# Kernel tuning notes

Hardware: AMD Instinct MI355X
Metric: run time of the kernel (lower is better)

## Reference

```python
import jax, jax.numpy as jnp
import numpy as np

T_TX, T_RX = 2, 2
NUM_VERTICES = 900
NUM_TRIANGLES = 400
ORDER = 2
NUM_PATH_CANDIDATES = 2048
EPSILON = 1e-6
HIT_THRESHOLD = 0.999


def setup_inputs() -> dict:
    key = jax.random.key(0)
    k1, k2, k3, k4, k5 = jax.random.split(key, 5)
    transmitters = jax.random.normal(k1, (T_TX, 3), dtype=jnp.float32) * 10.0
    receivers = jax.random.normal(k2, (T_RX, 3), dtype=jnp.float32) * 10.0
    vertices = jax.random.normal(k3, (NUM_VERTICES, 3), dtype=jnp.float32) * 5.0
    # Build triangles with three distinct vertex indices to avoid degenerate normals.
    i0 = jax.random.randint(k4, (NUM_TRIANGLES,), 0, NUM_VERTICES)
    triangles = jnp.stack([i0, (i0 + 7) % NUM_VERTICES, (i0 + 131) % NUM_VERTICES], axis=-1)
    tv = vertices[triangles]  # [Nt, 3, 3]
    n = jnp.cross(tv[:, 1] - tv[:, 0], tv[:, 2] - tv[:, 0])
    normals = n / jnp.linalg.norm(n, axis=-1, keepdims=True)  # unit plane normals, [Nt, 3]
    path_candidates = jax.random.randint(k5, (NUM_PATH_CANDIDATES, ORDER), 0, NUM_TRIANGLES)
    return {
        "transmitters": transmitters,
        "receivers": receivers,
        "vertices": vertices,
        "normals": normals,
        "triangles": triangles,
        "path_candidates": path_candidates,
    }


def image_method(from_v, to_v, mirror_vertices, mirror_normals):
    """from_v [T,1,1,3], to_v [1,R,1,3], mirrors [P,order,3] -> paths [T,R,P,order,3]."""
    num_mirrors = mirror_vertices.shape[-2]
    # Forward pass: successive mirror images of the transmitter.
    images = []
    cur = from_v
    for i in range(num_mirrors):
        mv = mirror_vertices[..., i, :]
        mn = mirror_normals[..., i, :]
        cur = cur - 2.0 * jnp.sum((cur - mv) * mn, axis=-1, keepdims=True) * mn
        images.append(cur)
    # Backward pass: intersect segment (image_i -> current point) with mirror plane i.
    pts = []
    cur = to_v
    for i in reversed(range(num_mirrors)):
        mv = mirror_vertices[..., i, :]
        mn = mirror_normals[..., i, :]
        img = images[i]
        u = cur - img
        t = jnp.sum((mv - img) * mn, axis=-1, keepdims=True) / jnp.sum(u * mn, axis=-1, keepdims=True)
        cur = img + t * u
        pts.append(cur)
    return jnp.stack(pts[::-1], axis=-2)


def triangles_contain_vertices(triangle_vertices, v):
    """triangle_vertices [P,order,3,3], v [T,R,P,order,3] -> bool [T,R,P,order]."""
    u0 = triangle_vertices[..., 0, :] - v
    u1 = triangle_vertices[..., 1, :] - v
    u2 = triangle_vertices[..., 2, :] - v
    n0 = jnp.cross(u0, u1)
    n1 = jnp.cross(u1, u2)
    n2 = jnp.cross(u2, u0)
    d01 = jnp.sum(n0 * n1, axis=-1)
    d12 = jnp.sum(n1 * n2, axis=-1)
    d20 = jnp.sum(n2 * n0, axis=-1)
    return (d01 >= 0.0) & (d12 >= 0.0) & (d20 >= 0.0)


def consecutive_same_side(full_paths, mirror_vertices, mirror_normals):
    """full_paths [T,R,P,order+2,3] -> bool [T,R,P,order]."""
    v_prev = full_paths[..., :-2, :]
    v_next = full_paths[..., 2:, :]
    d_prev = jnp.sum((v_prev - mirror_vertices) * mirror_normals, axis=-1)
    d_next = jnp.sum((v_next - mirror_vertices) * mirror_normals, axis=-1)
    return (d_prev * d_next) >= 0.0


def rays_intersect_any_triangle(ray_origins, ray_directions, triangle_vertices,
                                epsilon=EPSILON, hit_threshold=HIT_THRESHOLD):
    """Moller-Trumbore: rays [...,3] vs all triangles [Nt,3,3] -> bool [...]."""
    v0 = triangle_vertices[..., 0, :]
    e1 = triangle_vertices[..., 1, :] - v0
    e2 = triangle_vertices[..., 2, :] - v0
    ro = ray_origins[..., None, :]   # [..., Nt, 3] after broadcast
    rd = ray_directions[..., None, :]
    h = jnp.cross(rd, e2)
    a = jnp.sum(e1 * h, axis=-1)
    f = 1.0 / a
    s = ro - v0
    u = f * jnp.sum(s * h, axis=-1)
    q = jnp.cross(s, e1)
    v = f * jnp.sum(rd * q, axis=-1)
    t = f * jnp.sum(e2 * q, axis=-1)
    hit = (jnp.abs(a) > epsilon) & (u >= 0.0) & (u <= 1.0) & (v >= 0.0) \
        & (u + v <= 1.0) & (t > epsilon) & (t < hit_threshold)
    return hit.any(axis=-1)


def reference(transmitters, receivers, vertices, normals, triangles, path_candidates):
    from_v = transmitters.reshape(-1, 3)  # [T, 3]
    to_v = receivers.reshape(-1, 3)       # [R, 3]
    n_tx, n_rx = from_v.shape[0], to_v.shape[0]
    num_pc, order = path_candidates.shape

    tri = jnp.take(triangles, path_candidates, axis=0)          # [P, order, 3]
    triangle_vertices = jnp.take(vertices, tri, axis=0)          # [P, order, 3, 3]
    mirror_vertices = triangle_vertices[..., 0, :]               # [P, order, 3]
    mirror_normals = jnp.take(normals, path_candidates, axis=0)  # [P, order, 3]

    paths = image_method(from_v[:, None, None, :], to_v[None, :, None, :],
                         mirror_vertices, mirror_normals)        # [T,R,P,order,3]

    mask_1 = triangles_contain_vertices(triangle_vertices, paths).all(axis=-1)

    full_paths = jnp.concatenate(
        (
            jnp.broadcast_to(from_v[:, None, None, None, :], (n_tx, n_rx, num_pc, 1, 3)),
            paths,
            jnp.broadcast_to(to_v[None, :, None, None, :], (n_tx, n_rx, num_pc, 1, 3)),
        ),
        axis=-2,
    )  # [T,R,P,order+2,3]

    mask_2 = consecutive_same_side(full_paths, mirror_vertices, mirror_normals).all(axis=-1)

    ray_origins = full_paths[..., :-1, :]           # [T,R,P,order+1,3]
    ray_directions = jnp.diff(full_paths, axis=-2)  # [T,R,P,order+1,3]
    all_triangle_vertices = jnp.take(vertices, triangles, axis=0)  # [Nt,3,3]
    intersect = rays_intersect_any_triangle(ray_origins, ray_directions,
                                            all_triangle_vertices).any(axis=-1)
    mask_3 = ~intersect

    mask = mask_1 & mask_2 & mask_3  # [T,R,P]

    object_dtype = path_candidates.dtype
    tx_objects = jnp.broadcast_to(jnp.arange(n_tx, dtype=object_dtype)[:, None, None, None],
                                  (n_tx, n_rx, num_pc, 1))
    rx_objects = jnp.broadcast_to(jnp.arange(n_rx, dtype=object_dtype)[None, :, None, None],
                                  (n_tx, n_rx, num_pc, 1))
    pc = jnp.broadcast_to(path_candidates, (n_tx, n_rx, num_pc, order))
    objects = jnp.concatenate((tx_objects, pc, rx_objects), axis=-1)  # [T,R,P,order+2]

    return full_paths, objects, mask
```

## Files before the change

kernel.cpp:

```cpp
#include <hip/hip_runtime.h>

#pragma clang fp contract(off)

namespace {

constexpr int kT  = 2;
constexpr int kR  = 2;
constexpr int kP  = 2048;
constexpr int kNT = 400;
constexpr float kEps   = 1e-6f;
constexpr float kHitTh = 0.999f;

constexpr int kNumPaths  = kT * kR * kP;
constexpr int kFpFloats  = kNumPaths * 12;
constexpr int kObjFloats = kNumPaths * 4;

constexpr int kPathsPerBlock = 64;
constexpr int kBlocks = kNumPaths / kPathsPerBlock;

__device__ inline void cross3(const float a[3], const float b[3], float o[3]) {
    o[0] = a[1] * b[2] - a[2] * b[1];
    o[1] = a[2] * b[0] - a[0] * b[2];
    o[2] = a[0] * b[1] - a[1] * b[0];
}
__device__ inline float dot3(const float a[3], const float b[3]) {
    return a[0] * b[0] + a[1] * b[1] + a[2] * b[2];
}

__global__ __launch_bounds__(256)
void fused_kernel(const float* __restrict__ tx,
                  const float* __restrict__ rx,
                  const float* __restrict__ verts,
                  const float* __restrict__ normals,
                  const int*   __restrict__ tris,
                  const int*   __restrict__ pcs,
                  float*       __restrict__ out)
{
    __shared__ float sV0[kNT][3];
    __shared__ float sE1[kNT][3];
    __shared__ float sE2[kNT][3];
    __shared__ float sFp[kPathsPerBlock][12];
    __shared__ int   sQueue[kPathsPerBlock];
    __shared__ int   sCount;

    const int tid = threadIdx.x;
    if (tid == 0) sCount = 0;
    __syncthreads();

    if (tid < kPathsPerBlock) {
        const int L    = blockIdx.x * kPathsPerBlock + tid;
        const int tIdx = L / (kR * kP);
        const int rem  = L % (kR * kP);
        const int rIdx = rem / kP;
        const int p    = rem % kP;

        float fp[4][3];
        fp[0][0] = tx[3 * tIdx + 0]; fp[0][1] = tx[3 * tIdx + 1]; fp[0][2] = tx[3 * tIdx + 2];
        fp[3][0] = rx[3 * rIdx + 0]; fp[3][1] = rx[3 * rIdx + 1]; fp[3][2] = rx[3 * rIdx + 2];

        const int pcm[2] = { pcs[2 * p + 0], pcs[2 * p + 1] };

        float tv[2][3][3];
        float mn[2][3];
        #pragma unroll
        for (int m = 0; m < 2; ++m) {
            int tc = pcm[m];
            int i0 = tris[3 * tc + 0], i1 = tris[3 * tc + 1], i2 = tris[3 * tc + 2];
            #pragma unroll
            for (int c = 0; c < 3; ++c) {
                tv[m][0][c] = verts[3 * i0 + c];
                tv[m][1][c] = verts[3 * i1 + c];
                tv[m][2][c] = verts[3 * i2 + c];
                mn[m][c]    = normals[3 * tc + c];
            }
        }

        float img0[3], img1[3];
        {
            float diff[3];
            #pragma unroll
            for (int c = 0; c < 3; ++c) diff[c] = fp[0][c] - tv[0][0][c];
            float d0 = dot3(diff, mn[0]);
            #pragma unroll
            for (int c = 0; c < 3; ++c) img0[c] = fp[0][c] - 2.0f * d0 * mn[0][c];
            #pragma unroll
            for (int c = 0; c < 3; ++c) diff[c] = img0[c] - tv[1][0][c];
            float d1 = dot3(diff, mn[1]);
            #pragma unroll
            for (int c = 0; c < 3; ++c) img1[c] = img0[c] - 2.0f * d1 * mn[1][c];
        }
        {
            float u[3], w[3];
            #pragma unroll
            for (int c = 0; c < 3; ++c) u[c] = fp[3][c] - img1[c];
            #pragma unroll
            for (int c = 0; c < 3; ++c) w[c] = tv[1][0][c] - img1[c];
            float tpar = dot3(w, mn[1]) / dot3(u, mn[1]);
            #pragma unroll
            for (int c = 0; c < 3; ++c) fp[2][c] = img1[c] + tpar * u[c];
            #pragma unroll
            for (int c = 0; c < 3; ++c) u[c] = fp[2][c] - img0[c];
            #pragma unroll
            for (int c = 0; c < 3; ++c) w[c] = tv[0][0][c] - img0[c];
            tpar = dot3(w, mn[0]) / dot3(u, mn[0]);
            #pragma unroll
            for (int c = 0; c < 3; ++c) fp[1][c] = img0[c] + tpar * u[c];
        }

        bool mask1 = true;
        #pragma unroll
        for (int m = 0; m < 2; ++m) {
            float u0[3], u1[3], u2[3], n0[3], n1[3], n2[3];
            #pragma unroll
            for (int c = 0; c < 3; ++c) {
                u0[c] = tv[m][0][c] - fp[1 + m][c];
                u1[c] = tv[m][1][c] - fp[1 + m][c];
                u2[c] = tv[m][2][c] - fp[1 + m][c];
            }
            cross3(u0, u1, n0); cross3(u1, u2, n1); cross3(u2, u0, n2);
            float d01 = dot3(n0, n1), d12 = dot3(n1, n2), d20 = dot3(n2, n0);
            mask1 = mask1 && (d01 >= 0.0f) && (d12 >= 0.0f) && (d20 >= 0.0f);
        }

        bool mask2 = true;
        #pragma unroll
        for (int m = 0; m < 2; ++m) {
            float a[3], b[3];
            #pragma unroll
            for (int c = 0; c < 3; ++c) {
                a[c] = fp[m][c]     - tv[m][0][c];
                b[c] = fp[m + 2][c] - tv[m][0][c];
            }
            float dp = dot3(a, mn[m]);
            float dn = dot3(b, mn[m]);
            mask2 = mask2 && (dp * dn >= 0.0f);
        }

        float* fpOut = out + (size_t)L * 12;
        #pragma unroll
        for (int pt = 0; pt < 4; ++pt)
            #pragma unroll
            for (int c = 0; c < 3; ++c) {
                fpOut[pt * 3 + c] = fp[pt][c];
                sFp[tid][pt * 3 + c] = fp[pt][c];
            }
        float* objOut = out + kFpFloats + (size_t)L * 4;
        objOut[0] = (float)tIdx;
        objOut[1] = (float)pcm[0];
        objOut[2] = (float)pcm[1];
        objOut[3] = (float)rIdx;

        if (mask1 && mask2) {
            int slot = atomicAdd(&sCount, 1);
            sQueue[slot] = tid;
        } else {
            out[kFpFloats + kObjFloats + L] = 0.0f;
        }
    } else {
        for (int j = tid - kPathsPerBlock; j < kNT; j += 256 - kPathsPerBlock) {
            int i0 = tris[3 * j + 0], i1 = tris[3 * j + 1], i2 = tris[3 * j + 2];
            float ax = verts[3 * i0 + 0], ay = verts[3 * i0 + 1], az = verts[3 * i0 + 2];
            float bx = verts[3 * i1 + 0], by = verts[3 * i1 + 1], bz = verts[3 * i1 + 2];
            float cx = verts[3 * i2 + 0], cy = verts[3 * i2 + 1], cz = verts[3 * i2 + 2];
            sV0[j][0] = ax;      sV0[j][1] = ay;      sV0[j][2] = az;
            sE1[j][0] = bx - ax; sE1[j][1] = by - ay; sE1[j][2] = bz - az;
            sE2[j][0] = cx - ax; sE2[j][1] = cy - ay; sE2[j][2] = cz - az;
        }
    }
    __syncthreads();

    const int wave = tid >> 6;
    const int lane = tid & 63;
    const int cnt  = sCount;

    for (int k = wave; k < cnt; k += 4) {
        const int pl = sQueue[k];
        const int L  = blockIdx.x * kPathsPerBlock + pl;

        float pquad[4][3];
        #pragma unroll
        for (int pt = 0; pt < 4; ++pt)
            #pragma unroll
            for (int c = 0; c < 3; ++c)
                pquad[pt][c] = sFp[pl][pt * 3 + c];

        bool anyhit = false;
        #pragma unroll
        for (int s = 0; s < 3; ++s) {
            if (anyhit) break;
            float ro[3], rd[3];
            #pragma unroll
            for (int c = 0; c < 3; ++c) {
                ro[c] = pquad[s][c];
                rd[c] = pquad[s + 1][c] - pquad[s][c];
            }
            for (int jb = 0; jb < 7; ++jb) {
                const int j = jb * 64 + lane;
                const bool valid = (j < kNT);
                const int jj = valid ? j : 0;
                float v0[3] = { sV0[jj][0], sV0[jj][1], sV0[jj][2] };
                float e1[3] = { sE1[jj][0], sE1[jj][1], sE1[jj][2] };
                float e2[3] = { sE2[jj][0], sE2[jj][1], sE2[jj][2] };
                float h[3]; cross3(rd, e2, h);
                float a = dot3(e1, h);
                float f = 1.0f / a;
                float sv[3];
                #pragma unroll
                for (int c = 0; c < 3; ++c) sv[c] = ro[c] - v0[c];
                float uu = f * dot3(sv, h);
                float q[3]; cross3(sv, e1, q);
                float vv = f * dot3(rd, q);
                float tt = f * dot3(e2, q);
                bool hit = valid
                        && (fabsf(a) > kEps) && (uu >= 0.0f) && (uu <= 1.0f)
                        && (vv >= 0.0f) && (uu + vv <= 1.0f)
                        && (tt > kEps) && (tt < kHitTh);
                if (__any(hit ? 1 : 0)) { anyhit = true; break; }
            }
        }

        if (lane == 0) {
            out[kFpFloats + kObjFloats + L] = anyhit ? 0.0f : 1.0f;
        }
    }
}

}

extern "C" void kernel_launch(void* const* d_in, const int* in_sizes, int n_in,
                              void* d_out, int out_size, void* d_ws, size_t ws_size,
                              hipStream_t stream)
{
    const float* tx      = (const float*)d_in[0];
    const float* rx      = (const float*)d_in[1];
    const float* verts   = (const float*)d_in[2];
    const float* normals = (const float*)d_in[3];
    const int*   tris    = (const int*)d_in[4];
    const int*   pcs     = (const int*)d_in[5];
    float* out = (float*)d_out;

    hipLaunchKernelGGL(fused_kernel, dim3(kBlocks), dim3(256), 0, stream,
                       tx, rx, verts, normals, tris, pcs, out);
}
```

Baseline: 65.33 us.

## Test all three segments per triangle load and vectorize path outputs

The occlusion loop is reordered so each lane loads a triangle from shared memory once and tests all three ray segments against it, instead of reloading the triangles for each segment. Early exit now happens per 64-triangle batch across all segments rather than per segment. The per-path outputs are written with float4 stores instead of scalar stores. The loop swap cuts shared-memory traffic and the number of __any votes, but it loses the per-segment early exit, so some extra work may be done when the first segment already hits.

Result: no change. 66.47 us (+1.7%).

```diff
diff --git a/kernel.cpp b/kernel.cpp
--- a/kernel.cpp
+++ b/kernel.cpp
@@ -136,19 +136,17 @@
             mask2 = mask2 && (dp * dn >= 0.0f);
         }
 
-        float* fpOut = out + (size_t)L * 12;
+        float4* fpOut4 = reinterpret_cast<float4*>(out + (size_t)L * 12);
+        fpOut4[0] = make_float4(fp[0][0], fp[0][1], fp[0][2], fp[1][0]);
+        fpOut4[1] = make_float4(fp[1][1], fp[1][2], fp[2][0], fp[2][1]);
+        fpOut4[2] = make_float4(fp[2][2], fp[3][0], fp[3][1], fp[3][2]);
         #pragma unroll
         for (int pt = 0; pt < 4; ++pt)
             #pragma unroll
-            for (int c = 0; c < 3; ++c) {
-                fpOut[pt * 3 + c] = fp[pt][c];
+            for (int c = 0; c < 3; ++c)
                 sFp[tid][pt * 3 + c] = fp[pt][c];
-            }
-        float* objOut = out + kFpFloats + (size_t)L * 4;
-        objOut[0] = (float)tIdx;
-        objOut[1] = (float)pcm[0];
-        objOut[2] = (float)pcm[1];
-        objOut[3] = (float)rIdx;
+        float4* objOut4 = reinterpret_cast<float4*>(out + kFpFloats + (size_t)L * 4);
+        objOut4[0] = make_float4((float)tIdx, (float)pcm[0], (float)pcm[1], (float)rIdx);
 
         if (mask1 && mask2) {
             int slot = atomicAdd(&sCount, 1);
@@ -177,46 +175,42 @@
         const int pl = sQueue[k];
         const int L  = blockIdx.x * kPathsPerBlock + pl;
 
-        float pquad[4][3];
-        #pragma unroll
-        for (int pt = 0; pt < 4; ++pt)
-            #pragma unroll
-            for (int c = 0; c < 3; ++c)
-                pquad[pt][c] = sFp[pl][pt * 3 + c];
+        float ro[3][3], rd[3][3];
+        #pragma unroll
+        for (int s = 0; s < 3; ++s)
+            #pragma unroll
+            for (int c = 0; c < 3; ++c) {
+                ro[s][c] = sFp[pl][s * 3 + c];
+                rd[s][c] = sFp[pl][(s + 1) * 3 + c] - sFp[pl][s * 3 + c];
+            }
 
         bool anyhit = false;
-        #pragma unroll
-        for (int s = 0; s < 3; ++s) {
-            if (anyhit) break;
-            float ro[3], rd[3];
-            #pragma unroll
-            for (int c = 0; c < 3; ++c) {
-                ro[c] = pquad[s][c];
-                rd[c] = pquad[s + 1][c] - pquad[s][c];
-            }
-            for (int jb = 0; jb < 7; ++jb) {
-                const int j = jb * 64 + lane;
-                const bool valid = (j < kNT);
-                const int jj = valid ? j : 0;
-                float v0[3] = { sV0[jj][0], sV0[jj][1], sV0[jj][2] };
-                float e1[3] = { sE1[jj][0], sE1[jj][1], sE1[jj][2] };
-                float e2[3] = { sE2[jj][0], sE2[jj][1], sE2[jj][2] };
-                float h[3]; cross3(rd, e2, h);
+        for (int jb = 0; jb < 7; ++jb) {
+            const int j = jb * 64 + lane;
+            const bool valid = (j < kNT);
+            const int jj = valid ? j : 0;
+            float v0[3] = { sV0[jj][0], sV0[jj][1], sV0[jj][2] };
+            float e1[3] = { sE1[jj][0], sE1[jj][1], sE1[jj][2] };
+            float e2[3] = { sE2[jj][0], sE2[jj][1], sE2[jj][2] };
+
+            bool hit = false;
+            #pragma unroll
+            for (int s = 0; s < 3; ++s) {
+                float h[3]; cross3(rd[s], e2, h);
                 float a = dot3(e1, h);
                 float f = 1.0f / a;
                 float sv[3];
                 #pragma unroll
-                for (int c = 0; c < 3; ++c) sv[c] = ro[c] - v0[c];
+                for (int c = 0; c < 3; ++c) sv[c] = ro[s][c] - v0[c];
                 float uu = f * dot3(sv, h);
                 float q[3]; cross3(sv, e1, q);
-                float vv = f * dot3(rd, q);
+                float vv = f * dot3(rd[s], q);
                 float tt = f * dot3(e2, q);
-                bool hit = valid
-                        && (fabsf(a) > kEps) && (uu >= 0.0f) && (uu <= 1.0f)
-                        && (vv >= 0.0f) && (uu + vv <= 1.0f)
-                        && (tt > kEps) && (tt < kHitTh);
-                if (__any(hit ? 1 : 0)) { anyhit = true; break; }
-            }
+                hit = hit || ((fabsf(a) > kEps) && (uu >= 0.0f) && (uu <= 1.0f)
+                           && (vv >= 0.0f) && (uu + vv <= 1.0f)
+                           && (tt > kEps) && (tt < kHitTh));
+            }
+            if (__any((hit && valid) ? 1 : 0)) { anyhit = true; break; }
         }
 
         if (lane == 0) {
```
